# Kernel optimization log

Hardware: AMD Instinct MI355X
Metric: run time of the kernel (lower is better)

The kernel has to match this reference:

```python
import jax, jax.numpy as jnp
import numpy as np

N, D, H, K, STEPS = 100000, 384, 128, 5, 3


def setup_inputs() -> dict:
    key = jax.random.key(0)
    ks = jax.random.split(key, 5)
    emb = jax.random.normal(ks[0], (N, D), dtype=jnp.float32)
    qv = jax.random.normal(ks[1], (D,), dtype=jnp.float32)
    W1 = jax.random.normal(ks[2], (2 * D, H), dtype=jnp.float32) * (1.0 / np.sqrt(2 * D))
    b1 = jnp.zeros((H,), dtype=jnp.float32)
    W2 = jax.random.normal(ks[3], (H, K), dtype=jnp.float32) * (1.0 / np.sqrt(H))
    b2 = jnp.zeros((K,), dtype=jnp.float32)
    nbr = jax.random.randint(ks[4], (N, K), 0, N, dtype=jnp.int32)  # k-NN neighbor ids per node
    return {"emb": emb, "qv": qv, "W1": W1, "b1": b1, "W2": W2, "b2": b2, "nbr": nbr}


def _quantum_walk(emb, qv, W1, b1, W2, b2, nbr):
    n, k = nbr.shape
    # coin_net MLP on [emb_i ; q] -- independent of walk state, compute once.
    inp = jnp.concatenate([emb, jnp.broadcast_to(qv, (n, qv.shape[0]))], axis=1)  # [n, 2d]
    h = jax.nn.relu(inp @ W1 + b1)
    amps = h @ W2 + b2  # [n, k]

    anorm = jnp.linalg.norm(amps, axis=1)                      # [n]
    c = amps[:, :, None] * amps[:, None, :]                    # [n, k, k] outer product
    cnorm = jnp.linalg.norm(c.reshape(n, -1), axis=1)          # [n] Frobenius norm
    valid = (anorm > 0) & jnp.isfinite(anorm) & (cnorm > 0)
    # fallback coin: ones outer product normalized -> all entries 1/k (||ones_{k,k}||_F = k)
    uniform = jnp.full((k, k), 1.0 / k, dtype=amps.dtype)
    safe_cnorm = jnp.where(cnorm > 0, cnorm, 1.0)
    coins = jnp.where(valid[:, None, None], c / safe_cnorm[:, None, None], uniform)  # [n,k,k]

    init = jnp.full((n, k), 1.0 / np.sqrt(n * k), dtype=amps.dtype)
    cols = jnp.broadcast_to(jnp.arange(k), (n, k))

    def step(state, _):
        s_p = jnp.einsum('nkl,nl->nk', coins, state)                    # coin_i @ state_i
        new_state = jnp.zeros_like(state).at[nbr, cols].add(s_p)        # scatter to neighbor slots
        norm = jnp.linalg.norm(new_state)
        safe = jnp.where(norm > 0, norm, 1.0)
        state = jnp.where(norm > 0, new_state / safe, init)
        return state, None

    state, _ = jax.lax.scan(step, init, None, length=STEPS)
    return jnp.abs(state).sum(axis=1)  # per-node retrieval logits [n]


def reference(emb, qv, W1, b1, W2, b2, nbr):
    return _quantum_walk(emb, qv, W1, b1, W2, b2, nbr)
```

## Files before the change

kernel.cpp:

```cpp
#include <hip/hip_runtime.h>
#include <hip/hip_bf16.h>
#include <math.h>

#define NN 100000
#define DD 384
#define HH 128
#define KK 5

typedef __attribute__((ext_vector_type(8))) short short8;
typedef __attribute__((ext_vector_type(4))) float f32x4;

constexpr float INIT_VAL = 1.4142135623730951e-3f;
constexpr float RSQRT5   = 0.44721359549995793f;

__device__ __forceinline__ void split_bf16(float x, ushort& hi, ushort& lo) {
    unsigned xb = __float_as_uint(x);
    hi = (ushort)(xb >> 16);
    float hif = __uint_as_float(((unsigned)hi) << 16);
    lo = (ushort)(__float_as_uint(x - hif) >> 16);
}

__device__ __forceinline__ void split8(float4 x, float4 y, short8& h, short8& l) {
    union { short8 s; unsigned u[4]; } H, L;
    float f[8] = {x.x, x.y, x.z, x.w, y.x, y.y, y.z, y.w};
#pragma unroll
    for (int d = 0; d < 4; ++d) {
        unsigned b0 = __float_as_uint(f[2 * d]);
        unsigned b1 = __float_as_uint(f[2 * d + 1]);
        H.u[d] = (b0 >> 16) | (b1 & 0xFFFF0000u);
        float l0 = f[2 * d]     - __uint_as_float(b0 & 0xFFFF0000u);
        float l1 = f[2 * d + 1] - __uint_as_float(b1 & 0xFFFF0000u);
        L.u[d] = (__float_as_uint(l0) >> 16) | (__float_as_uint(l1) & 0xFFFF0000u);
    }
    h = H.s;
    l = L.s;
}

typedef __attribute__((address_space(3))) unsigned lds_as_t;
typedef __attribute__((address_space(1))) const unsigned glb_as_t;
__device__ __forceinline__ void gload_lds16(const float* g, float* l) {
    __builtin_amdgcn_global_load_lds((glb_as_t*)g, (lds_as_t*)l, 16, 0, 0);
}

__global__ __launch_bounds__(256) void prep_kernel(
    const float* __restrict__ qv, const float* __restrict__ W1,
    const float* __restrict__ b1, const int* __restrict__ nbr,
    float* __restrict__ b1p, ushort* __restrict__ W1h, ushort* __restrict__ W1l,
    int* __restrict__ nbrT, float* __restrict__ sA, float* __restrict__ sB,
    float* __restrict__ sC, float* __restrict__ ssp) {
    const int b = blockIdx.x, tid = threadIdx.x;
    if (b == 0) {
        if (tid == 0) ssp[0] = 0.f;
        if (tid < HH) {
            float s = b1[tid];
#pragma unroll 16
            for (int k = 0; k < DD; ++k)
                s = fmaf(qv[k], W1[(size_t)(DD + k) * HH + tid], s);
            b1p[tid] = s;
        }
    } else if (b <= 24) {
        int t = (b - 1) * 256 + tid;
        int l = t & 63;
        int ks = (t >> 6) % 12;
        int c = (t >> 6) / 12;
        int k0 = ks * 32 + ((l >> 4) << 3);
        int col = c * 16 + (l & 15);
#pragma unroll
        for (int e = 0; e < 8; ++e) {
            ushort hv, lv;
            split_bf16(W1[(size_t)(k0 + e) * HH + col], hv, lv);
            W1h[(size_t)t * 8 + e] = hv;
            W1l[(size_t)t * 8 + e] = lv;
        }
    } else {
        int i = (b - 25) * 256 + tid;
        if (i < NN) {
#pragma unroll
            for (int j = 0; j < KK; ++j) {
                nbrT[j * NN + i] = nbr[i * KK + j];
                sA[j * NN + i] = 0.f;
                sB[j * NN + i] = 0.f;
                sC[j * NN + i] = 0.f;
            }
        }
    }
}

__global__ __launch_bounds__(256, 2) void mlp_mfma_kernel(
    const float* __restrict__ emb, const ushort* __restrict__ W1h,
    const ushort* __restrict__ W1l, const float* __restrict__ b1p,
    const float* __restrict__ W2, const float* __restrict__ b2,
    const int* __restrict__ nbrT, float* __restrict__ gout ,
    float* __restrict__ sA) {
    __shared__ __align__(16) float Abuf[2][64][128];
    __shared__ float pbuf[64][2][8];

    const int tid = threadIdx.x;
    const int lane = tid & 63;
    const int wid = tid >> 6;
    const int wm = wid >> 1;
    const int wn = wid & 1;
    const int blkBase = blockIdx.x * 64;

    const int lrow = lane >> 5;
    const int lc16 = lane & 31;

    auto stage = [&](int buf, int t) {
        const int kbase = t * 128;
#pragma unroll
        for (int s = 0; s < 8; ++s) {
            int rl = wid * 16 + s * 2;
            int r = rl + lrow;
            int node = min(blkBase + r, NN - 1);
            int sb = (lc16 * 16) ^ ((r & 31) << 4);
            gload_lds16(emb + (size_t)node * DD + kbase + (sb >> 2), &Abuf[buf][rl][0]);
        }
    };

    f32x4 acc[2][4];
#pragma unroll
    for (int mt = 0; mt < 2; ++mt)
#pragma unroll
        for (int nt = 0; nt < 4; ++nt) acc[mt][nt] = (f32x4){0.f, 0.f, 0.f, 0.f};

    stage(0, 0);
    __syncthreads();

#pragma unroll
    for (int t = 0; t < 3; ++t) {
        if (t < 2) stage((t + 1) & 1, t + 1);
        const int buf = t & 1;

        short8 bh[2][4], bl[2][4];
        auto loadB = [&](int kt, int sb2) {
            int ks = t * 4 + kt;
#pragma unroll
            for (int nt = 0; nt < 4; ++nt) {
                size_t off = ((size_t)((wn * 4 + nt) * 12 + ks) * 64 + lane) * 8;
                bh[sb2][nt] = *reinterpret_cast<const short8*>(&W1h[off]);
                bl[sb2][nt] = *reinterpret_cast<const short8*>(&W1l[off]);
            }
        };
        loadB(0, 0);
#pragma unroll
        for (int kt = 0; kt < 4; ++kt) {
            const int cur = kt & 1, nxt = cur ^ 1;
            if (kt < 3) loadB(kt + 1, nxt);
            short8 ah[2], al[2];
#pragma unroll
            for (int mt = 0; mt < 2; ++mt) {
                int row = wm * 32 + mt * 16 + (lane & 15);
                int c0 = kt * 128 + ((lane >> 4) << 5);
                int sw = (row & 31) << 4;
                const char* base = (const char*)(&Abuf[buf][row][0]);
                float4 x = *(const float4*)(base + (c0 ^ sw));
                float4 y = *(const float4*)(base + ((c0 + 16) ^ sw));
                split8(x, y, ah[mt], al[mt]);
            }
#pragma unroll
            for (int nt = 0; nt < 4; ++nt) {
                acc[0][nt] = __builtin_amdgcn_mfma_f32_16x16x32_bf16(ah[0], bh[cur][nt], acc[0][nt], 0, 0, 0);
                acc[1][nt] = __builtin_amdgcn_mfma_f32_16x16x32_bf16(ah[1], bh[cur][nt], acc[1][nt], 0, 0, 0);
            }
#pragma unroll
            for (int nt = 0; nt < 4; ++nt) {
                acc[0][nt] = __builtin_amdgcn_mfma_f32_16x16x32_bf16(al[0], bh[cur][nt], acc[0][nt], 0, 0, 0);
                acc[1][nt] = __builtin_amdgcn_mfma_f32_16x16x32_bf16(al[1], bh[cur][nt], acc[1][nt], 0, 0, 0);
            }
#pragma unroll
            for (int nt = 0; nt < 4; ++nt) {
                acc[0][nt] = __builtin_amdgcn_mfma_f32_16x16x32_bf16(ah[0], bl[cur][nt], acc[0][nt], 0, 0, 0);
                acc[1][nt] = __builtin_amdgcn_mfma_f32_16x16x32_bf16(ah[1], bl[cur][nt], acc[1][nt], 0, 0, 0);
            }
        }
        __syncthreads();
    }

    float b1v[4], w2v[4][KK];
#pragma unroll
    for (int nt = 0; nt < 4; ++nt) {
        int h = wn * 64 + nt * 16 + (lane & 15);
        b1v[nt] = b1p[h];
#pragma unroll
        for (int j = 0; j < KK; ++j) w2v[nt][j] = W2[h * KK + j];
    }
#pragma unroll
    for (int mt = 0; mt < 2; ++mt) {
        float p[4][KK];
#pragma unroll
        for (int r = 0; r < 4; ++r)
#pragma unroll
            for (int j = 0; j < KK; ++j) p[r][j] = 0.f;
#pragma unroll
        for (int nt = 0; nt < 4; ++nt)
#pragma unroll
            for (int r = 0; r < 4; ++r) {
                float v = fmaxf(acc[mt][nt][r] + b1v[nt], 0.f);
#pragma unroll
                for (int j = 0; j < KK; ++j) p[r][j] = fmaf(v, w2v[nt][j], p[r][j]);
            }
#pragma unroll
        for (int off = 1; off < 16; off <<= 1)
#pragma unroll
            for (int r = 0; r < 4; ++r)
#pragma unroll
                for (int j = 0; j < KK; ++j) p[r][j] += __shfl_xor(p[r][j], off, 64);
        if ((lane & 15) == 0) {
            int rowbase = wm * 32 + mt * 16 + (lane >> 4) * 4;
#pragma unroll
            for (int r = 0; r < 4; ++r)
#pragma unroll
                for (int j = 0; j < KK; ++j) pbuf[rowbase + r][wn][j] = p[r][j];
        }
    }
    __syncthreads();
    if (tid < 64) {
        int node = blkBase + tid;
        float a[KK], an2 = 0.f;
#pragma unroll
        for (int j = 0; j < KK; ++j) {
            a[j] = pbuf[tid][0][j] + pbuf[tid][1][j] + b2[j];
            an2 = fmaf(a[j], a[j], an2);
        }
        float an = sqrtf(an2);
        bool valid = (an2 > 0.f) && isfinite(an);
        if (node < NN) {
            float g5[KK], ssum = 0.f;
#pragma unroll
            for (int j = 0; j < KK; ++j) {
                g5[j] = valid ? (a[j] / an) : RSQRT5;
                gout[j * NN + node] = g5[j];
                ssum += g5[j];
            }
            float d = ssum * INIT_VAL;
#pragma unroll
            for (int j = 0; j < KK; ++j)
                atomicAdd(&sA[j * NN + nbrT[j * NN + node]], g5[j] * d);
        }
    }
}

__global__ void walk_step_kernel(const float* __restrict__ g, const int* __restrict__ nbrT,
                                 const float* __restrict__ u, float* __restrict__ v) {
    int i = blockIdx.x * blockDim.x + threadIdx.x;
    if (i >= NN) return;
    float gj[KK], d = 0.f;
#pragma unroll
    for (int j = 0; j < KK; ++j) {
        gj[j] = g[j * NN + i];
        d = fmaf(gj[j], u[j * NN + i], d);
    }
#pragma unroll
    for (int j = 0; j < KK; ++j)
        atomicAdd(&v[j * NN + nbrT[j * NN + i]], gj[j] * d);
}

__global__ void norm_reduce_kernel(const float* __restrict__ u, float* __restrict__ ss) {
    int i = blockIdx.x * blockDim.x + threadIdx.x;
    const int total4 = (KK * NN) / 4;
    float s = 0.f;
    for (int idx = i; idx < total4; idx += gridDim.x * blockDim.x) {
        float4 x = reinterpret_cast<const float4*>(u)[idx];
        s = fmaf(x.x, x.x, s);
        s = fmaf(x.y, x.y, s);
        s = fmaf(x.z, x.z, s);
        s = fmaf(x.w, x.w, s);
    }
#pragma unroll
    for (int off = 32; off > 0; off >>= 1) s += __shfl_xor(s, off, 64);
    if ((threadIdx.x & 63) == 0) atomicAdd(ss, s);
}

__global__ void finalize_kernel(const float* __restrict__ u, const float* __restrict__ ss,
                                float* __restrict__ out) {
    int i = blockIdx.x * blockDim.x + threadIdx.x;
    if (i >= NN) return;
    float s = 0.f;
#pragma unroll
    for (int j = 0; j < KK; ++j) s += fabsf(u[j * NN + i]);
    float nrm = sqrtf(*ss);
    out[i] = (nrm > 0.f) ? (s / nrm) : (KK * INIT_VAL);
}

extern "C" void kernel_launch(void* const* d_in, const int* in_sizes, int n_in,
                              void* d_out, int out_size, void* d_ws, size_t ws_size,
                              hipStream_t stream) {
    const float* emb = (const float*)d_in[0];
    const float* qv  = (const float*)d_in[1];
    const float* W1  = (const float*)d_in[2];
    const float* b1  = (const float*)d_in[3];
    const float* W2  = (const float*)d_in[4];
    const float* b2  = (const float*)d_in[5];
    const int*   nbr = (const int*)d_in[6];
    float* out = (float*)d_out;

    char* ws = (char*)d_ws;
    size_t off = 0;
    auto alloc = [&](size_t bytes) {
        char* p = ws + off;
        off += (bytes + 255) & ~(size_t)255;
        return p;
    };
    float*  b1p  = (float*)alloc(HH * sizeof(float));
    ushort* W1h  = (ushort*)alloc((size_t)DD * HH * sizeof(ushort));
    ushort* W1l  = (ushort*)alloc((size_t)DD * HH * sizeof(ushort));
    float*  gbuf = (float*)alloc((size_t)KK * NN * sizeof(float));
    int*    nbrT = (int*)  alloc((size_t)KK * NN * sizeof(int));
    float*  sA   = (float*)alloc((size_t)KK * NN * sizeof(float));
    float*  sB   = (float*)alloc((size_t)KK * NN * sizeof(float));
    float*  sC   = (float*)alloc((size_t)KK * NN * sizeof(float));
    float*  ssp  = (float*)alloc(sizeof(float));

    const int nblk = (NN + 255) / 256;

    prep_kernel<<<25 + nblk, 256, 0, stream>>>(qv, W1, b1, nbr, b1p, W1h, W1l,
                                               nbrT, sA, sB, sC, ssp);
    mlp_mfma_kernel<<<(NN + 63) / 64, 256, 0, stream>>>(emb, W1h, W1l, b1p, W2, b2,
                                                        nbrT, gbuf, sA);

    walk_step_kernel<<<nblk, 256, 0, stream>>>(gbuf, nbrT, sA, sB);
    walk_step_kernel<<<nblk, 256, 0, stream>>>(gbuf, nbrT, sB, sC);

    norm_reduce_kernel<<<512, 256, 0, stream>>>(sC, ssp);
    finalize_kernel<<<nblk, 256, 0, stream>>>(sC, ssp, out);
}
```

Measured before the change: 173.4 us.

## Load emb rows directly into registers, drop LDS staging, use 32-row blocks

The MLP kernel stops staging emb tiles through LDS with global_load_lds and double buffering. Each lane now loads its whole 384-float row slice into registers up front, and the block tile shrinks from 64 to 32 nodes, one 16-row M-tile per wave. This removes the LDS round trip, the swizzle arithmetic and the block barriers, and launches twice as many blocks. In exchange it costs about 96 VGPRs per lane for the A fragments, drops the occupancy hint, and assumes NN divides evenly by 32 because the bounds checks were removed.

Result: slower. 185.9 us (+7.2%).

```diff
diff --git a/kernel.cpp b/kernel.cpp
--- a/kernel.cpp
+++ b/kernel.cpp
@@ -34,12 +34,6 @@
     }
     h = H.s;
     l = L.s;
-}
-
-typedef __attribute__((address_space(3))) unsigned lds_as_t;
-typedef __attribute__((address_space(1))) const unsigned glb_as_t;
-__device__ __forceinline__ void gload_lds16(const float* g, float* l) {
-    __builtin_amdgcn_global_load_lds((glb_as_t*)g, (lds_as_t*)l, 16, 0, 0);
 }
 
 __global__ __launch_bounds__(256) void prep_kernel(
@@ -86,95 +80,76 @@
     }
 }
 
-__global__ __launch_bounds__(256, 2) void mlp_mfma_kernel(
+__global__ __launch_bounds__(256) void mlp_mfma_kernel(
     const float* __restrict__ emb, const ushort* __restrict__ W1h,
     const ushort* __restrict__ W1l, const float* __restrict__ b1p,
     const float* __restrict__ W2, const float* __restrict__ b2,
     const int* __restrict__ nbrT, float* __restrict__ gout ,
     float* __restrict__ sA) {
-    __shared__ __align__(16) float Abuf[2][64][128];
-    __shared__ float pbuf[64][2][8];
+    __shared__ float pbuf[32][2][8];
 
     const int tid = threadIdx.x;
     const int lane = tid & 63;
     const int wid = tid >> 6;
     const int wm = wid >> 1;
     const int wn = wid & 1;
-    const int blkBase = blockIdx.x * 64;
-
-    const int lrow = lane >> 5;
-    const int lc16 = lane & 31;
-
-    auto stage = [&](int buf, int t) {
-        const int kbase = t * 128;
-#pragma unroll
-        for (int s = 0; s < 8; ++s) {
-            int rl = wid * 16 + s * 2;
-            int r = rl + lrow;
-            int node = min(blkBase + r, NN - 1);
-            int sb = (lc16 * 16) ^ ((r & 31) << 4);
-            gload_lds16(emb + (size_t)node * DD + kbase + (sb >> 2), &Abuf[buf][rl][0]);
+    const int blkBase = blockIdx.x * 32;
+    const int nb = blkBase + wm * 16;
+
+    const float* ap = emb + (size_t)(nb + (lane & 15)) * DD + ((lane >> 4) << 3);
+
+    float4 aF[12][2];
+#pragma unroll
+    for (int ks = 0; ks < 12; ++ks) {
+        aF[ks][0] = *reinterpret_cast<const float4*>(ap + ks * 32);
+        aF[ks][1] = *reinterpret_cast<const float4*>(ap + ks * 32 + 4);
+    }
+
+    short8 bh[2][4], bl[2][4];
+    auto loadB = [&](int ks, int buf) {
+#pragma unroll
+        for (int nt = 0; nt < 4; ++nt) {
+            size_t off = ((size_t)((wn * 4 + nt) * 12 + ks) * 64 + lane) * 8;
+            bh[buf][nt] = *reinterpret_cast<const short8*>(&W1h[off]);
+            bl[buf][nt] = *reinterpret_cast<const short8*>(&W1l[off]);
         }
     };
 
-    f32x4 acc[2][4];
-#pragma unroll
-    for (int mt = 0; mt < 2; ++mt)
-#pragma unroll
-        for (int nt = 0; nt < 4; ++nt) acc[mt][nt] = (f32x4){0.f, 0.f, 0.f, 0.f};
-
-    stage(0, 0);
-    __syncthreads();
-
-#pragma unroll
-    for (int t = 0; t < 3; ++t) {
-        if (t < 2) stage((t + 1) & 1, t + 1);
-        const int buf = t & 1;
-
-        short8 bh[2][4], bl[2][4];
-        auto loadB = [&](int kt, int sb2) {
-            int ks = t * 4 + kt;
-#pragma unroll
-            for (int nt = 0; nt < 4; ++nt) {
-                size_t off = ((size_t)((wn * 4 + nt) * 12 + ks) * 64 + lane) * 8;
-                bh[sb2][nt] = *reinterpret_cast<const short8*>(&W1h[off]);
-                bl[sb2][nt] = *reinterpret_cast<const short8*>(&W1l[off]);
-            }
-        };
-        loadB(0, 0);
-#pragma unroll
-        for (int kt = 0; kt < 4; ++kt) {
-            const int cur = kt & 1, nxt = cur ^ 1;
-            if (kt < 3) loadB(kt + 1, nxt);
-            short8 ah[2], al[2];
-#pragma unroll
-            for (int mt = 0; mt < 2; ++mt) {
-                int row = wm * 32 + mt * 16 + (lane & 15);
-                int c0 = kt * 128 + ((lane >> 4) << 5);
-                int sw = (row & 31) << 4;
-                const char* base = (const char*)(&Abuf[buf][row][0]);
-                float4 x = *(const float4*)(base + (c0 ^ sw));
-                float4 y = *(const float4*)(base + ((c0 + 16) ^ sw));
-                split8(x, y, ah[mt], al[mt]);
-            }
-#pragma unroll
-            for (int nt = 0; nt < 4; ++nt) {
-                acc[0][nt] = __builtin_amdgcn_mfma_f32_16x16x32_bf16(ah[0], bh[cur][nt], acc[0][nt], 0, 0, 0);
-                acc[1][nt] = __builtin_amdgcn_mfma_f32_16x16x32_bf16(ah[1], bh[cur][nt], acc[1][nt], 0, 0, 0);
-            }
-#pragma unroll
-            for (int nt = 0; nt < 4; ++nt) {
-                acc[0][nt] = __builtin_amdgcn_mfma_f32_16x16x32_bf16(al[0], bh[cur][nt], acc[0][nt], 0, 0, 0);
-                acc[1][nt] = __builtin_amdgcn_mfma_f32_16x16x32_bf16(al[1], bh[cur][nt], acc[1][nt], 0, 0, 0);
-            }
-#pragma unroll
-            for (int nt = 0; nt < 4; ++nt) {
-                acc[0][nt] = __builtin_amdgcn_mfma_f32_16x16x32_bf16(ah[0], bl[cur][nt], acc[0][nt], 0, 0, 0);
-                acc[1][nt] = __builtin_amdgcn_mfma_f32_16x16x32_bf16(ah[1], bl[cur][nt], acc[1][nt], 0, 0, 0);
-            }
-        }
-        __syncthreads();
-    }
+    f32x4 acc[4];
+#pragma unroll
+    for (int nt = 0; nt < 4; ++nt) acc[nt] = (f32x4){0.f, 0.f, 0.f, 0.f};
+
+    loadB(0, 0);
+
+#define QW_STEP(KS, CUR, NXT)                                                        \
+    {                                                                                \
+        if ((KS) < 11) loadB((KS) + 1, (NXT));                                       \
+        short8 ah, al;                                                               \
+        split8(aF[KS][0], aF[KS][1], ah, al);                                        \
+        _Pragma("unroll")                                                            \
+        for (int nt = 0; nt < 4; ++nt)                                               \
+            acc[nt] = __builtin_amdgcn_mfma_f32_16x16x32_bf16(ah, bh[CUR][nt], acc[nt], 0, 0, 0); \
+        _Pragma("unroll")                                                            \
+        for (int nt = 0; nt < 4; ++nt)                                               \
+            acc[nt] = __builtin_amdgcn_mfma_f32_16x16x32_bf16(al, bh[CUR][nt], acc[nt], 0, 0, 0); \
+        _Pragma("unroll")                                                            \
+        for (int nt = 0; nt < 4; ++nt)                                               \
+            acc[nt] = __builtin_amdgcn_mfma_f32_16x16x32_bf16(ah, bl[CUR][nt], acc[nt], 0, 0, 0); \
+    }
+
+    QW_STEP(0, 0, 1)
+    QW_STEP(1, 1, 0)
+    QW_STEP(2, 0, 1)
+    QW_STEP(3, 1, 0)
+    QW_STEP(4, 0, 1)
+    QW_STEP(5, 1, 0)
+    QW_STEP(6, 0, 1)
+    QW_STEP(7, 1, 0)
+    QW_STEP(8, 0, 1)
+    QW_STEP(9, 1, 0)
+    QW_STEP(10, 0, 1)
+    QW_STEP(11, 1, 0)
+#undef QW_STEP
 
     float b1v[4], w2v[4][KK];
 #pragma unroll
@@ -184,37 +159,34 @@
 #pragma unroll
         for (int j = 0; j < KK; ++j) w2v[nt][j] = W2[h * KK + j];
     }
-#pragma unroll
-    for (int mt = 0; mt < 2; ++mt) {
-        float p[4][KK];
+    float p[4][KK];
+#pragma unroll
+    for (int r = 0; r < 4; ++r)
+#pragma unroll
+        for (int j = 0; j < KK; ++j) p[r][j] = 0.f;
+#pragma unroll
+    for (int nt = 0; nt < 4; ++nt)
+#pragma unroll
+        for (int r = 0; r < 4; ++r) {
+            float v = fmaxf(acc[nt][r] + b1v[nt], 0.f);
+#pragma unroll
+            for (int j = 0; j < KK; ++j) p[r][j] = fmaf(v, w2v[nt][j], p[r][j]);
+        }
+#pragma unroll
+    for (int off = 1; off < 16; off <<= 1)
 #pragma unroll
         for (int r = 0; r < 4; ++r)
 #pragma unroll
-            for (int j = 0; j < KK; ++j) p[r][j] = 0.f;
-#pragma unroll
-        for (int nt = 0; nt < 4; ++nt)
-#pragma unroll
-            for (int r = 0; r < 4; ++r) {
-                float v = fmaxf(acc[mt][nt][r] + b1v[nt], 0.f);
-#pragma unroll
-                for (int j = 0; j < KK; ++j) p[r][j] = fmaf(v, w2v[nt][j], p[r][j]);
-            }
-#pragma unroll
-        for (int off = 1; off < 16; off <<= 1)
-#pragma unroll
-            for (int r = 0; r < 4; ++r)
-#pragma unroll
-                for (int j = 0; j < KK; ++j) p[r][j] += __shfl_xor(p[r][j], off, 64);
-        if ((lane & 15) == 0) {
-            int rowbase = wm * 32 + mt * 16 + (lane >> 4) * 4;
-#pragma unroll
-            for (int r = 0; r < 4; ++r)
-#pragma unroll
-                for (int j = 0; j < KK; ++j) pbuf[rowbase + r][wn][j] = p[r][j];
-        }
+            for (int j = 0; j < KK; ++j) p[r][j] += __shfl_xor(p[r][j], off, 64);
+    if ((lane & 15) == 0) {
+        int rowbase = wm * 16 + (lane >> 4) * 4;
+#pragma unroll
+        for (int r = 0; r < 4; ++r)
+#pragma unroll
+            for (int j = 0; j < KK; ++j) pbuf[rowbase + r][wn][j] = p[r][j];
     }
     __syncthreads();
-    if (tid < 64) {
+    if (tid < 32) {
         int node = blkBase + tid;
         float a[KK], an2 = 0.f;
 #pragma unroll
@@ -224,19 +196,17 @@
         }
         float an = sqrtf(an2);
         bool valid = (an2 > 0.f) && isfinite(an);
-        if (node < NN) {
-            float g5[KK], ssum = 0.f;
-#pragma unroll
-            for (int j = 0; j < KK; ++j) {
-                g5[j] = valid ? (a[j] / an) : RSQRT5;
-                gout[j * NN + node] = g5[j];
-                ssum += g5[j];
-            }
-            float d = ssum * INIT_VAL;
-#pragma unroll
-            for (int j = 0; j < KK; ++j)
-                atomicAdd(&sA[j * NN + nbrT[j * NN + node]], g5[j] * d);
-        }
+        float g5[KK], ssum = 0.f;
+#pragma unroll
+        for (int j = 0; j < KK; ++j) {
+            g5[j] = valid ? (a[j] / an) : RSQRT5;
+            gout[j * NN + node] = g5[j];
+            ssum += g5[j];
+        }
+        float d = ssum * INIT_VAL;
+#pragma unroll
+        for (int j = 0; j < KK; ++j)
+            atomicAdd(&sA[j * NN + nbrT[j * NN + node]], g5[j] * d);
     }
 }
 
@@ -315,8 +285,8 @@
 
     prep_kernel<<<25 + nblk, 256, 0, stream>>>(qv, W1, b1, nbr, b1p, W1h, W1l,
                                                nbrT, sA, sB, sC, ssp);
-    mlp_mfma_kernel<<<(NN + 63) / 64, 256, 0, stream>>>(emb, W1h, W1l, b1p, W2, b2,
-                                                        nbrT, gbuf, sA);
+    mlp_mfma_kernel<<<NN / 32, 256, 0, stream>>>(emb, W1h, W1l, b1p, W2, b2,
+                                                 nbrT, gbuf, sA);
 
     walk_step_kernel<<<nblk, 256, 0, stream>>>(gbuf, nbrT, sA, sB);
     walk_step_kernel<<<nblk, 256, 0, stream>>>(gbuf, nbrT, sB, sC);
```
